# Performance work log

Hardware: AMD Instinct MI355X
Metric: run time of the kernel (lower is better)

Reference implementation:

```python
import jax, jax.numpy as jnp
import numpy as np

DIM_INPUT = 100000
DIM_LATENT = 128
NNZ = 819200
BATCH = 16384


def setup_inputs() -> dict:
    key = jax.random.key(0)
    k1, k2, k3, k4, k5 = jax.random.split(key, 5)
    vals = jax.random.uniform(k1, (NNZ,), dtype=jnp.float32)
    row_idx = jnp.sort(jax.random.randint(k2, (NNZ,), 0, BATCH, dtype=jnp.int32))
    col_idx = jax.random.randint(k3, (NNZ,), 0, DIM_INPUT, dtype=jnp.int32)
    # learned parameters (match torch init: w0 zeros, w/v randn)
    w0 = jnp.zeros((1,), dtype=jnp.float32)
    w = jax.random.normal(k4, (DIM_INPUT,), dtype=jnp.float32)
    v = jax.random.normal(k5, (DIM_INPUT, DIM_LATENT), dtype=jnp.float32)
    return {"vals": vals, "row_idx": row_idx, "col_idx": col_idx,
            "batch": BATCH, "w0": w0, "w": w, "v": v}


def reference(vals, row_idx, col_idx, batch, w0, w, v):
    # x is a sparse [batch, dim_input] matrix in COO form (row_idx, col_idx, vals).
    # linear term: w0 + x @ w
    linear = w0[0] + jax.ops.segment_sum(vals * w[col_idx], row_idx,
                                         num_segments=batch)
    # gather latent rows once: [nnz, K]
    v_rows = v[col_idx]
    weighted = vals[:, None] * v_rows                      # [nnz, K]
    xv = jax.ops.segment_sum(weighted, row_idx, num_segments=batch)       # [B, K]
    x_v_sq = jax.ops.segment_sum(weighted * v_rows, row_idx,
                                 num_segments=batch)       # x @ (v**2): [B, K]
    interaction = 0.5 * (jnp.sum(xv * xv, axis=1) - jnp.sum(x_v_sq, axis=1))
    return linear + interaction
```

## Files before the change

### kernel.cpp

```cpp
#include <hip/hip_runtime.h>

#define FM_NNZ   819200
#define FM_BATCH 16384
#define FM_K     128

__global__ __launch_bounds__(128) void fm_fwd_kernel(
    const float* __restrict__ vals,
    const int*   __restrict__ row_idx,
    const int*   __restrict__ col_idx,
    const float* __restrict__ w0,
    const float* __restrict__ w,
    const float* __restrict__ v,
    float*       __restrict__ out)
{
    const int row = blockIdx.x;
    const int k   = threadIdx.x;

    int lo = 0, hi = FM_NNZ;
    while (lo < hi) {
        int mid = (lo + hi) >> 1;
        if (row_idx[mid] < row) lo = mid + 1; else hi = mid;
    }
    const int start = lo;
    hi = FM_NNZ;
    while (lo < hi) {
        int mid = (lo + hi) >> 1;
        if (row_idx[mid] < row + 1) lo = mid + 1; else hi = mid;
    }
    const int end = lo;

    float xv = 0.0f;
    float sq = 0.0f;
    #pragma unroll 4
    for (int i = start; i < end; ++i) {
        const float val = vals[i];
        const int   col = col_idx[i];
        const float vk  = v[(size_t)col * FM_K + k];
        const float t   = val * vk;
        xv += t;
        sq = fmaf(t, vk, sq);
    }

    float lin = 0.0f;
    for (int i = start + k; i < end; i += FM_K) {
        lin = fmaf(vals[i], w[col_idx[i]], lin);
    }

    float local = fmaf(xv, xv, -sq);
    #pragma unroll
    for (int off = 32; off > 0; off >>= 1) {
        local += __shfl_down(local, off);
        lin   += __shfl_down(lin, off);
    }
    __shared__ float s_local[2], s_lin[2];
    const int wave = threadIdx.x >> 6;
    if ((threadIdx.x & 63) == 0) { s_local[wave] = local; s_lin[wave] = lin; }
    __syncthreads();
    if (threadIdx.x == 0) {
        const float inter = 0.5f * (s_local[0] + s_local[1]);
        const float linear = s_lin[0] + s_lin[1];
        out[row] = w0[0] + linear + inter;
    }
}

extern "C" void kernel_launch(void* const* d_in, const int* in_sizes, int n_in,
                              void* d_out, int out_size, void* d_ws, size_t ws_size,
                              hipStream_t stream) {
    const float* vals    = (const float*)d_in[0];
    const int*   row_idx = (const int*)  d_in[1];
    const int*   col_idx = (const int*)  d_in[2];
    const float* w0      = (const float*)d_in[4];
    const float* w       = (const float*)d_in[5];
    const float* v       = (const float*)d_in[6];
    float*       out     = (float*)d_out;

    fm_fwd_kernel<<<FM_BATCH, FM_K, 0, stream>>>(vals, row_idx, col_idx, w0, w, v, out);
}
```

Before: 180.1 us.

## Map one wave per row with float2 gathers and shuffle-broadcast indices

Each 64-lane wave now handles one batch row, and each lane owns two latent dimensions through float2 loads of v. Column indices and values are loaded cooperatively once per 64-entry chunk and broadcast with shuffles. Up to eight v-row gathers are issued before they are consumed, which raises memory-level parallelism. The linear term is folded into the same pass, and the shared-memory and __syncthreads block reduction is removed in favour of a wave-level shuffle reduction. Blocks now hold four rows each, so the per-row binary searches run per wave.

```diff
diff --git a/kernel.cpp b/kernel.cpp
--- a/kernel.cpp
+++ b/kernel.cpp
@@ -3,8 +3,10 @@
 #define FM_NNZ   819200
 #define FM_BATCH 16384
 #define FM_K     128
+#define WAVES    4
+#define BATCH8   8
 
-__global__ __launch_bounds__(128) void fm_fwd_kernel(
+__global__ __launch_bounds__(256) void fm_fwd_kernel(
     const float* __restrict__ vals,
     const int*   __restrict__ row_idx,
     const int*   __restrict__ col_idx,
@@ -13,8 +15,9 @@
     const float* __restrict__ v,
     float*       __restrict__ out)
 {
-    const int row = blockIdx.x;
-    const int k   = threadIdx.x;
+    const int wave = threadIdx.x >> 6;
+    const int lane = threadIdx.x & 63;
+    const int row  = blockIdx.x * WAVES + wave;
 
     int lo = 0, hi = FM_NNZ;
     while (lo < hi) {
@@ -29,37 +32,60 @@
     }
     const int end = lo;
 
-    float xv = 0.0f;
-    float sq = 0.0f;
-    #pragma unroll 4
-    for (int i = start; i < end; ++i) {
-        const float val = vals[i];
-        const int   col = col_idx[i];
-        const float vk  = v[(size_t)col * FM_K + k];
-        const float t   = val * vk;
-        xv += t;
-        sq = fmaf(t, vk, sq);
+    const float2* __restrict__ v2 = (const float2*)v;
+
+    float2 xv = make_float2(0.f, 0.f);
+    float2 sq = make_float2(0.f, 0.f);
+    float  lin = 0.f;
+
+    for (int base = start; base < end; base += 64) {
+        const int cnt = min(64, end - base);
+
+        const int idxc = min(base + lane, FM_NNZ - 1);
+        const int   c  = col_idx[idxc];
+        const float a  = (lane < cnt) ? vals[idxc] : 0.f;
+
+        lin = fmaf(a, w[c], lin);
+
+        int j = 0;
+        for (; j + BATCH8 <= cnt; j += BATCH8) {
+            float2 vv[BATCH8];
+            float  aa[BATCH8];
+            #pragma unroll
+            for (int u = 0; u < BATCH8; ++u) {
+                const int   cj = __shfl(c, j + u);
+                aa[u] = __shfl(a, j + u);
+                vv[u] = v2[(size_t)cj * 64 + lane];
+            }
+            #pragma unroll
+            for (int u = 0; u < BATCH8; ++u) {
+                const float tx = aa[u] * vv[u].x;
+                const float ty = aa[u] * vv[u].y;
+                xv.x += tx;  xv.y += ty;
+                sq.x = fmaf(tx, vv[u].x, sq.x);
+                sq.y = fmaf(ty, vv[u].y, sq.y);
+            }
+        }
+        for (; j < cnt; ++j) {
+            const int   cj = __shfl(c, j);
+            const float aj = __shfl(a, j);
+            const float2 vvj = v2[(size_t)cj * 64 + lane];
+            const float tx = aj * vvj.x;
+            const float ty = aj * vvj.y;
+            xv.x += tx;  xv.y += ty;
+            sq.x = fmaf(tx, vvj.x, sq.x);
+            sq.y = fmaf(ty, vvj.y, sq.y);
+        }
     }
 
-    float lin = 0.0f;
-    for (int i = start + k; i < end; i += FM_K) {
-        lin = fmaf(vals[i], w[col_idx[i]], lin);
-    }
-
-    float local = fmaf(xv, xv, -sq);
+    float part = xv.x * xv.x + xv.y * xv.y - sq.x - sq.y;
     #pragma unroll
     for (int off = 32; off > 0; off >>= 1) {
-        local += __shfl_down(local, off);
-        lin   += __shfl_down(lin, off);
+        part += __shfl_down(part, off);
+        lin  += __shfl_down(lin,  off);
     }
-    __shared__ float s_local[2], s_lin[2];
-    const int wave = threadIdx.x >> 6;
-    if ((threadIdx.x & 63) == 0) { s_local[wave] = local; s_lin[wave] = lin; }
-    __syncthreads();
-    if (threadIdx.x == 0) {
-        const float inter = 0.5f * (s_local[0] + s_local[1]);
-        const float linear = s_lin[0] + s_lin[1];
-        out[row] = w0[0] + linear + inter;
+    if (lane == 0) {
+        out[row] = w0[0] + lin + 0.5f * part;
     }
 }
 
@@ -74,5 +100,6 @@
     const float* v       = (const float*)d_in[6];
     float*       out     = (float*)d_out;
 
-    fm_fwd_kernel<<<FM_BATCH, FM_K, 0, stream>>>(vals, row_idx, col_idx, w0, w, v, out);
+    fm_fwd_kernel<<<FM_BATCH / WAVES, 64 * WAVES, 0, stream>>>(
+        vals, row_idx, col_idx, w0, w, v, out);
 }
```

New measurement: 170.4 us. -5.4%, faster.
